# Kernel optimization log

Hardware: AMD Instinct MI355X
Metric: run time of the kernel (lower is better)

Reference implementation:

```python
import jax, jax.numpy as jnp
import numpy as np

NH = 8      # num_heads
KP = 3      # propagation_steps

def _ln(x, g, b, eps=1e-5):
    m = jnp.mean(x, -1, keepdims=True)
    v = jnp.mean(jnp.square(x - m), -1, keepdims=True)
    return (x - m) * jax.lax.rsqrt(v + eps) * g + b

def _mha(x, Wq, bq, Wk, bk, Wv, bv, Wo, bo):
    B, L, H = x.shape
    dh = H // NH
    q = (x @ Wq + bq).reshape(B, L, NH, dh)
    k = (x @ Wk + bk).reshape(B, L, NH, dh)
    v = (x @ Wv + bv).reshape(B, L, NH, dh)
    s = jnp.einsum('blhd,bmhd->bhlm', q, k) / jnp.sqrt(jnp.asarray(dh, x.dtype))
    p = jax.nn.softmax(s, axis=-1)
    o = jnp.einsum('bhlm,bmhd->blhd', p, v).reshape(B, L, H)
    return o @ Wo + bo

def setup_inputs():
    B, S, N, H = 2, 12, 800, 64
    keys = jax.random.split(jax.random.key(0), 64)
    it = iter(range(64))
    def nk():
        return keys[next(it)]
    def w(shape):
        return jax.random.normal(nk(), shape, jnp.float32) * 0.02
    p = {}
    p['x'] = jax.random.normal(nk(), (B, S, N, H), jnp.float32)
    # uniform weights scaled by 1/N (~row-normalized dense adjacency)
    p['adj'] = jax.random.uniform(nk(), (B, N, N), jnp.float32) / N
    p['W_gp'] = w((H, H)); p['b_gp'] = jnp.zeros((H,), jnp.float32)
    for sfx in ('s', 't'):
        for nm in ('Wq', 'Wk', 'Wv', 'Wo'):
            p[nm + '_' + sfx] = w((H, H))
        for nm in ('bq', 'bk', 'bv', 'bo'):
            p[nm + '_' + sfx] = jnp.zeros((H,), jnp.float32)
        p['g_' + sfx] = jnp.ones((H,), jnp.float32)
        p['be_' + sfx] = jnp.zeros((H,), jnp.float32)
    p['W1'] = w((H, 4 * H)); p['b1'] = jnp.zeros((4 * H,), jnp.float32)
    p['W2'] = w((4 * H, H)); p['b2'] = jnp.zeros((H,), jnp.float32)
    p['g1'] = jnp.ones((H,), jnp.float32); p['be1'] = jnp.zeros((H,), jnp.float32)
    p['g2'] = jnp.ones((H,), jnp.float32); p['be2'] = jnp.zeros((H,), jnp.float32)
    return p

def reference(x, adj, W_gp, b_gp,
              Wq_s, Wk_s, Wv_s, Wo_s, bq_s, bk_s, bv_s, bo_s, g_s, be_s,
              Wq_t, Wk_t, Wv_t, Wo_t, bq_t, bk_t, bv_t, bo_t, g_t, be_t,
              W1, b1, W2, b2, g1, be1, g2, be2):
    B, S, N, H = x.shape
    residual = x
    # accident-aware scaling (hidden_dim >= 6 path)
    acc = x[..., -2] * jnp.exp(-x[..., -1] / 60.0)
    xs = x * (1.0 + 0.3 * acc[..., None])
    # graph propagation: linear then K steps of relu(A @ h), vectorized over time
    h = xs @ W_gp + b_gp
    for _ in range(KP):
        h = jax.nn.relu(jnp.einsum('bnm,bsmh->bsnh', adj, h))
    prop = h + residual
    # spatial attention over nodes within each timestep
    xsa = prop.reshape(B * S, N, H)
    a = _mha(xsa, Wq_s, bq_s, Wk_s, bk_s, Wv_s, bv_s, Wo_s, bo_s)
    a = _ln(a + xsa, g_s, be_s).reshape(B, S, N, H)
    # temporal attention over timesteps per node
    xta = a.transpose(0, 2, 1, 3).reshape(B * N, S, H)
    t = _mha(xta, Wq_t, bq_t, Wk_t, bk_t, Wv_t, bv_t, Wo_t, bo_t)
    t = _ln(t + xta, g_t, be_t).reshape(B, N, S, H).transpose(0, 2, 1, 3)
    attn_out = t
    # pre-norm FFN with residual, post-norm output
    f = _ln(attn_out, g1, be1)
    f = jax.nn.relu(f @ W1 + b1) @ W2 + b2
    f = f + attn_out
    return _ln(f, g2, be2)
```

## Files before the change

kernel.cpp:

```cpp
#include <hip/hip_runtime.h>
#include <hip/hip_bf16.h>

#define NB 2
#define NS 12
#define NN 800
#define HEADS 8
#define DH 8
#define NBS (NB*NS)
#define NR (NB*NS*NN)

typedef __attribute__((ext_vector_type(4))) float f32x4;
typedef __attribute__((ext_vector_type(4))) short s16x4;
typedef __attribute__((ext_vector_type(8))) short s16x8;

static __device__ __forceinline__ unsigned short f2bf(float f) {
  union { float f; unsigned u; } v; v.f = f;
  unsigned r = (v.u + 0x7FFFu + ((v.u >> 16) & 1u)) >> 16;
  return (unsigned short)r;
}
static __device__ __forceinline__ float bf2f(unsigned short u) {
  union { unsigned u; float f; } v;
  v.u = ((unsigned)u) << 16;
  return v.f;
}
static __device__ __forceinline__ float fexp2(float x) {
  return __builtin_amdgcn_exp2f(x);
}
static __device__ __forceinline__ unsigned cvtpk_bf16(float a, float b) {
  unsigned r;
  asm("v_cvt_pk_bf16_f32 %0, %1, %2" : "=v"(r) : "v"(a), "v"(b));
  return r;
}

#define SC_LOG2 (0.35355339059327373f * 1.44269504088896f)

__global__ __launch_bounds__(256) void k_wconv(
    const float* __restrict__ w0, const float* __restrict__ w1,
    const float* __restrict__ w2, const float* __restrict__ w3,
    const float* __restrict__ w4, const float* __restrict__ w5,
    const float* __restrict__ w6, const float* __restrict__ w7,
    const float* __restrict__ w8, const float* __restrict__ W1,
    const float* __restrict__ W2, unsigned short* __restrict__ WB,
    unsigned short* __restrict__ W1B, unsigned short* __restrict__ W2B) {
  int i = blockIdx.x * 256 + threadIdx.x;
  if (i < 36864) {
    const float* ws[9] = {w0, w1, w2, w3, w4, w5, w6, w7, w8};
    WB[i] = f2bf(ws[i >> 12][i & 4095]);
  } else if (i < 53248) {
    W1B[i - 36864] = f2bf(W1[i - 36864]);
  } else if (i < 69632) {
    W2B[i - 53248] = f2bf(W2[i - 53248]);
  }
}

__global__ __launch_bounds__(256) void k_lin64T(
    const float* __restrict__ x, const unsigned short* __restrict__ Wb,
    const float* __restrict__ bias, unsigned short* __restrict__ HP) {
  __shared__ unsigned short As[32][36];
  __shared__ unsigned short Bs[64][36];
  const int tid = threadIdx.x;
  const int r0 = blockIdx.x * 32;
  const int w = tid >> 6, l = tid & 63;
  const int rb = (w & 1) * 16, cb = (w >> 1) * 32;
  f32x4 acc0 = {0.f, 0.f, 0.f, 0.f}, acc1 = {0.f, 0.f, 0.f, 0.f};
  const int ar = tid >> 3, ak = (tid & 7) * 4;
  const int bc = tid & 63, bm0 = (tid >> 6) * 4;
  const int k4 = (l >> 4) * 4;
  const int arow = rb + (l & 15);
  const int bcol0 = cb + (l & 15);
  const float* xrow = x + (size_t)(r0 + ar) * 64;
  float sf = 1.0f + 0.3f * xrow[62] * __expf(-xrow[63] * (1.0f / 60.0f));
  for (int k0 = 0; k0 < 64; k0 += 32) {
    __syncthreads();
    float4 xv = *(const float4*)(xrow + k0 + ak);
    ushort4 xb;
    xb.x = f2bf(xv.x * sf); xb.y = f2bf(xv.y * sf);
    xb.z = f2bf(xv.z * sf); xb.w = f2bf(xv.w * sf);
    *(ushort4*)&As[ar][ak] = xb;
#pragma unroll
    for (int j = 0; j < 4; ++j) {
      int mp = bm0 + j;
      unsigned lo = Wb[(size_t)(k0 + 2 * mp) * 64 + bc];
      unsigned hi = Wb[(size_t)(k0 + 2 * mp + 1) * 64 + bc];
      *(unsigned*)&Bs[bc][2 * mp] = lo | (hi << 16);
    }
    __syncthreads();
    s16x4 alo = *(const s16x4*)&As[arow][k4];
    s16x4 ahi = *(const s16x4*)&As[arow][k4 + 16];
    s16x8 a = {alo.x, alo.y, alo.z, alo.w, ahi.x, ahi.y, ahi.z, ahi.w};
    s16x4 b0l = *(const s16x4*)&Bs[bcol0][k4];
    s16x4 b0h = *(const s16x4*)&Bs[bcol0][k4 + 16];
    s16x8 bf0 = {b0l.x, b0l.y, b0l.z, b0l.w, b0h.x, b0h.y, b0h.z, b0h.w};
    s16x4 b1l = *(const s16x4*)&Bs[bcol0 + 16][k4];
    s16x4 b1h = *(const s16x4*)&Bs[bcol0 + 16][k4 + 16];
    s16x8 bf1 = {b1l.x, b1l.y, b1l.z, b1l.w, b1h.x, b1h.y, b1h.z, b1h.w};
    acc0 = __builtin_amdgcn_mfma_f32_16x16x32_bf16(a, bf0, acc0, 0, 0, 0);
    acc1 = __builtin_amdgcn_mfma_f32_16x16x32_bf16(a, bf1, acc1, 0, 0, 0);
  }
  const int c0 = cb + (l & 15);
  float b0 = bias[c0], b1 = bias[c0 + 16];
#pragma unroll
  for (int r = 0; r < 4; ++r) {
    int row = r0 + rb + (l >> 4) * 4 + r;
    int bs = row / NN, m = row % NN;
    HP[((size_t)bs * 64 + c0) * NN + m] = f2bf(acc0[r] + b0);
    HP[((size_t)bs * 64 + c0 + 16) * NN + m] = f2bf(acc1[r] + b1);
  }
}

template <bool LAST>
__global__ __launch_bounds__(256) void k_prop_mfma(
    const float* __restrict__ adj,
    const unsigned short* __restrict__ HPin,
    const float* __restrict__ x,
    unsigned short* __restrict__ HPout,
    float* __restrict__ pout,
    unsigned short* __restrict__ pbout) {
  __shared__ unsigned short As[32][36];
  __shared__ unsigned short Bs[64][40];
  const int tid = threadIdx.x;
  const int bid = blockIdx.x;
  const int bs = bid / 25, mt = bid % 25;
  const int b = bs / NS;
  const int n0 = mt * 32;
  const float* abase = adj + (size_t)b * NN * NN + (size_t)n0 * NN;
  const unsigned short* hbase = HPin + (size_t)bs * 64 * NN;
  const int w = tid >> 6, l = tid & 63;
  const int rb = (w & 1) * 16;
  const int cb = (w >> 1) * 32;
  f32x4 acc0 = {0.f, 0.f, 0.f, 0.f}, acc1 = {0.f, 0.f, 0.f, 0.f};
  const int ar = tid >> 3, ak = (tid & 7) * 4;
  const int bc = tid & 63, bq = tid >> 6;
  const int k4 = (l >> 4) * 4;
  const int arow = rb + (l & 15);
  const int bcol0 = cb + (l & 15);
  float4 av = *(const float4*)(abase + (size_t)ar * NN + ak);
  s16x8 bv = *(const s16x8*)(hbase + (size_t)bc * NN + bq * 8);
  for (int m0 = 0; m0 < NN; m0 += 32) {
    __syncthreads();
    {
      ushort4 ab;
      ab.x = f2bf(av.x); ab.y = f2bf(av.y);
      ab.z = f2bf(av.z); ab.w = f2bf(av.w);
      *(ushort4*)&As[ar][ak] = ab;
      *(s16x8*)&Bs[bc][bq * 8] = bv;
    }
    __syncthreads();
    if (m0 + 32 < NN) {
      av = *(const float4*)(abase + (size_t)ar * NN + m0 + 32 + ak);
      bv = *(const s16x8*)(hbase + (size_t)bc * NN + m0 + 32 + bq * 8);
    }
    s16x4 alo = *(const s16x4*)&As[arow][k4];
    s16x4 ahi = *(const s16x4*)&As[arow][k4 + 16];
    s16x8 a = {alo.x, alo.y, alo.z, alo.w, ahi.x, ahi.y, ahi.z, ahi.w};
    s16x4 b0l = *(const s16x4*)&Bs[bcol0][k4];
    s16x4 b0h = *(const s16x4*)&Bs[bcol0][k4 + 16];
    s16x8 bf0 = {b0l.x, b0l.y, b0l.z, b0l.w, b0h.x, b0h.y, b0h.z, b0h.w};
    s16x4 b1l = *(const s16x4*)&Bs[bcol0 + 16][k4];
    s16x4 b1h = *(const s16x4*)&Bs[bcol0 + 16][k4 + 16];
    s16x8 bf1 = {b1l.x, b1l.y, b1l.z, b1l.w, b1h.x, b1h.y, b1h.z, b1h.w};
    acc0 = __builtin_amdgcn_mfma_f32_16x16x32_bf16(a, bf0, acc0, 0, 0, 0);
    acc1 = __builtin_amdgcn_mfma_f32_16x16x32_bf16(a, bf1, acc1, 0, 0, 0);
  }
  const int c0 = cb + (l & 15);
  if (LAST) {
#pragma unroll
    for (int r = 0; r < 4; ++r) {
      int n = n0 + rb + (l >> 4) * 4 + r;
      float v0 = fmaxf(acc0[r], 0.f);
      float v1 = fmaxf(acc1[r], 0.f);
      size_t i0 = ((size_t)bs * NN + n) * 64 + c0;
      size_t i1 = i0 + 16;
      float p0 = v0 + x[i0], p1 = v1 + x[i1];
      pout[i0] = p0;
      pout[i1] = p1;
      pbout[i0] = f2bf(p0);
      pbout[i1] = f2bf(p1);
    }
  } else {
    int nb = n0 + rb + (l >> 4) * 4;
    s16x4 o0, o1;
#pragma unroll
    for (int r = 0; r < 4; ++r) {
      o0[r] = (short)f2bf(fmaxf(acc0[r], 0.f));
      o1[r] = (short)f2bf(fmaxf(acc1[r], 0.f));
    }
    *(s16x4*)&HPout[((size_t)bs * 64 + c0) * NN + nb] = o0;
    *(s16x4*)&HPout[((size_t)bs * 64 + c0 + 16) * NN + nb] = o1;
  }
}

__global__ __launch_bounds__(256) void k_qkv_mfma(
    const unsigned short* __restrict__ Xb,
    const unsigned short* __restrict__ Wq,
    const unsigned short* __restrict__ Wk,
    const unsigned short* __restrict__ Wv,
    const float* __restrict__ bq, const float* __restrict__ bk,
    const float* __restrict__ bv, float qscale,
    unsigned short* __restrict__ Qo, unsigned short* __restrict__ Ko,
    unsigned short* __restrict__ Vo) {
  __shared__ unsigned short As[32][36];
  __shared__ unsigned short Bs[3][64][36];
  const int tid = threadIdx.x;
  const int r0 = blockIdx.x * 32;
  const int w = tid >> 6, l = tid & 63;
  const int rb = (w & 1) * 16;
  const int cb = (w >> 1) * 32;
  f32x4 acc[3][2];
#pragma unroll
  for (int i = 0; i < 3; ++i)
#pragma unroll
    for (int j = 0; j < 2; ++j) acc[i][j] = (f32x4){0.f, 0.f, 0.f, 0.f};
  const unsigned short* Wm[3] = {Wq, Wk, Wv};
  const int ar = tid >> 3, ak = (tid & 7) * 4;
  const int bc = tid & 63, bm0 = (tid >> 6) * 4;
  const int k4 = (l >> 4) * 4;
  const int arow = rb + (l & 15);
  const int bcol0 = cb + (l & 15);
  for (int k0 = 0; k0 < 64; k0 += 32) {
    __syncthreads();
    *(s16x4*)&As[ar][ak] =
        *(const s16x4*)(Xb + (size_t)(r0 + ar) * 64 + k0 + ak);
#pragma unroll
    for (int wm = 0; wm < 3; ++wm) {
#pragma unroll
      for (int j = 0; j < 4; ++j) {
        int mp = bm0 + j;
        unsigned lo = Wm[wm][(size_t)(k0 + 2 * mp) * 64 + bc];
        unsigned hi = Wm[wm][(size_t)(k0 + 2 * mp + 1) * 64 + bc];
        *(unsigned*)&Bs[wm][bc][2 * mp] = lo | (hi << 16);
      }
    }
    __syncthreads();
    s16x4 alo = *(const s16x4*)&As[arow][k4];
    s16x4 ahi = *(const s16x4*)&As[arow][k4 + 16];
    s16x8 a = {alo.x, alo.y, alo.z, alo.w, ahi.x, ahi.y, ahi.z, ahi.w};
#pragma unroll
    for (int wm = 0; wm < 3; ++wm) {
      s16x4 b0l = *(const s16x4*)&Bs[wm][bcol0][k4];
      s16x4 b0h = *(const s16x4*)&Bs[wm][bcol0][k4 + 16];
      s16x8 bf0 = {b0l.x, b0l.y, b0l.z, b0l.w, b0h.x, b0h.y, b0h.z, b0h.w};
      s16x4 b1l = *(const s16x4*)&Bs[wm][bcol0 + 16][k4];
      s16x4 b1h = *(const s16x4*)&Bs[wm][bcol0 + 16][k4 + 16];
      s16x8 bf1 = {b1l.x, b1l.y, b1l.z, b1l.w, b1h.x, b1h.y, b1h.z, b1h.w};
      acc[wm][0] = __builtin_amdgcn_mfma_f32_16x16x32_bf16(a, bf0, acc[wm][0], 0, 0, 0);
      acc[wm][1] = __builtin_amdgcn_mfma_f32_16x16x32_bf16(a, bf1, acc[wm][1], 0, 0, 0);
    }
  }
  const float* bm[3] = {bq, bk, bv};
  unsigned short* Om[3] = {Qo, Ko, Vo};
  const int c0 = cb + (l & 15);
#pragma unroll
  for (int wm = 0; wm < 3; ++wm) {
    float b0 = bm[wm][c0], b1 = bm[wm][c0 + 16];
    float sc = (wm == 0) ? qscale : 1.0f;
#pragma unroll
    for (int r = 0; r < 4; ++r) {
      int row = r0 + rb + (l >> 4) * 4 + r;
      Om[wm][(size_t)row * 64 + c0] = f2bf((acc[wm][0][r] + b0) * sc);
      Om[wm][(size_t)row * 64 + c0 + 16] = f2bf((acc[wm][1][r] + b1) * sc);
    }
  }
}

__global__ __launch_bounds__(256) void k_sattn5(
    const unsigned short* __restrict__ Qb,
    const unsigned short* __restrict__ Kb,
    const unsigned short* __restrict__ Vb,
    unsigned short* __restrict__ OB) {
  __shared__ unsigned short Ks[800][8];
  __shared__ unsigned short Vt[25 * 256 + 256];
  const int bs = blockIdx.x, h = blockIdx.y;
  const int tid = threadIdx.x;
  const size_t base = (size_t)bs * NN * 64 + h * DH;
  for (int r = tid; r < NN; r += 256)
    *(s16x8*)&Ks[r][0] = *(const s16x8*)(Kb + base + (size_t)r * 64);
  if (tid < 200) {
    int t = tid >> 3, c = tid & 7;
    int r = t * 32 + c * 4;
    s16x8 v0 = *(const s16x8*)(Vb + base + (size_t)r * 64);
    s16x8 v1 = *(const s16x8*)(Vb + base + (size_t)(r + 1) * 64);
    s16x8 v2 = *(const s16x8*)(Vb + base + (size_t)(r + 2) * 64);
    s16x8 v3 = *(const s16x8*)(Vb + base + (size_t)(r + 3) * 64);
#pragma unroll
    for (int d = 0; d < 8; ++d) {
      unsigned lo = (unsigned short)v0[d] | ((unsigned)(unsigned short)v1[d] << 16);
      unsigned hi = (unsigned short)v2[d] | ((unsigned)(unsigned short)v3[d] << 16);
      unsigned* dst = (unsigned*)&Vt[t * 256 + d * 32 + ((c ^ d) & 7) * 4];
      dst[0] = lo;
      dst[1] = hi;
    }
  }
  __syncthreads();
  const int w = tid >> 6, l = tid & 63;
  const int q0 = blockIdx.z * 128 + w * 32;
  if (q0 >= NN) return;
  const int r15 = l & 15, g = l >> 4;
  const int dd = r15;
  const int off1 = dd * 32 + ((g ^ dd) & 7) * 4;
  const int off2 = dd * 32 + (((4 + g) ^ dd) & 7) * 4;
  s16x4 qvA = *(const s16x4*)(Qb + base + (size_t)(q0 + r15) * 64 + (g & 1) * 4);
  s16x4 qvB = *(const s16x4*)(Qb + base + (size_t)(q0 + 16 + r15) * 64 + (g & 1) * 4);
  s16x8 qfA = {0, 0, 0, 0, 0, 0, 0, 0};
  s16x8 qfB = {0, 0, 0, 0, 0, 0, 0, 0};
  if (g < 2) {
    qfA[0] = qvA.x; qfA[1] = qvA.y; qfA[2] = qvA.z; qfA[3] = qvA.w;
    qfB[0] = qvB.x; qfB[1] = qvB.y; qfB[2] = qvB.z; qfB[3] = qvB.w;
  }
  const short one_bf = (short)0x3F80;
  f32x4 accA = {0.f, 0.f, 0.f, 0.f}, accB = {0.f, 0.f, 0.f, 0.f};
  const f32x4 zero4 = {0.f, 0.f, 0.f, 0.f};
#pragma unroll 5
  for (int t = 0; t < 25; ++t) {
    s16x4 ka = *(const s16x4*)&Ks[t * 32 + r15][(g & 1) * 4];
    s16x4 kb = *(const s16x4*)&Ks[t * 32 + 16 + r15][(g & 1) * 4];
    s16x8 kfa = {0, 0, 0, 0, 0, 0, 0, 0};
    s16x8 kfb = {0, 0, 0, 0, 0, 0, 0, 0};
    if (g < 2) {
      kfa[0] = ka.x; kfa[1] = ka.y; kfa[2] = ka.z; kfa[3] = ka.w;
      kfb[0] = kb.x; kfb[1] = kb.y; kfb[2] = kb.z; kfb[3] = kb.w;
    }
    s16x4 va = *(const s16x4*)&Vt[t * 256 + off1];
    s16x4 vb = *(const s16x4*)&Vt[t * 256 + off2];
    s16x8 vf;
    if (dd < 8) {
      vf = (s16x8){va.x, va.y, va.z, va.w, vb.x, vb.y, vb.z, vb.w};
    } else if (dd == 8) {
      vf = (s16x8){one_bf, one_bf, one_bf, one_bf, one_bf, one_bf, one_bf, one_bf};
    } else {
      vf = (s16x8){0, 0, 0, 0, 0, 0, 0, 0};
    }
    f32x4 sA1 = __builtin_amdgcn_mfma_f32_16x16x32_bf16(kfa, qfA, zero4, 0, 0, 0);
    f32x4 sA2 = __builtin_amdgcn_mfma_f32_16x16x32_bf16(kfb, qfA, zero4, 0, 0, 0);
    f32x4 sB1 = __builtin_amdgcn_mfma_f32_16x16x32_bf16(kfa, qfB, zero4, 0, 0, 0);
    f32x4 sB2 = __builtin_amdgcn_mfma_f32_16x16x32_bf16(kfb, qfB, zero4, 0, 0, 0);
    float pA[8], pB[8];
#pragma unroll
    for (int r = 0; r < 4; ++r) {
      pA[r] = fexp2(sA1[r]);
      pA[4 + r] = fexp2(sA2[r]);
      pB[r] = fexp2(sB1[r]);
      pB[4 + r] = fexp2(sB2[r]);
    }
    union { unsigned u[4]; s16x8 v; } puA, puB;
    puA.u[0] = cvtpk_bf16(pA[0], pA[1]);
    puA.u[1] = cvtpk_bf16(pA[2], pA[3]);
    puA.u[2] = cvtpk_bf16(pA[4], pA[5]);
    puA.u[3] = cvtpk_bf16(pA[6], pA[7]);
    puB.u[0] = cvtpk_bf16(pB[0], pB[1]);
    puB.u[1] = cvtpk_bf16(pB[2], pB[3]);
    puB.u[2] = cvtpk_bf16(pB[4], pB[5]);
    puB.u[3] = cvtpk_bf16(pB[6], pB[7]);
    accA = __builtin_amdgcn_mfma_f32_16x16x32_bf16(vf, puA.v, accA, 0, 0, 0);
    accB = __builtin_amdgcn_mfma_f32_16x16x32_bf16(vf, puB.v, accB, 0, 0, 0);
  }
  float lsA = __shfl(accA[0], 32 + r15, 64);
  float lsB = __shfl(accB[0], 32 + r15, 64);
  float invA = 1.f / lsA;
  float invB = 1.f / lsB;
  if (g < 2) {
#pragma unroll
    for (int r = 0; r < 4; ++r) {
      int d = g * 4 + r;
      OB[base + (size_t)(q0 + r15) * 64 + d] = f2bf(accA[r] * invA);
      OB[base + (size_t)(q0 + 16 + r15) * 64 + d] = f2bf(accB[r] * invB);
    }
  }
}

template <bool LN2>
__global__ __launch_bounds__(256) void k_projln_mfma(
    const unsigned short* __restrict__ Xb,
    const unsigned short* __restrict__ Wb,
    const float* __restrict__ bias, const float* __restrict__ res,
    const float* __restrict__ g, const float* __restrict__ be,
    const float* __restrict__ g2, const float* __restrict__ be2,
    float* __restrict__ out, unsigned short* __restrict__ bfout) {
  __shared__ unsigned short As[32][36];
  __shared__ unsigned short Bs[64][36];
  __shared__ float CT[32][68];
  const int tid = threadIdx.x;
  const int r0 = blockIdx.x * 32;
  const int w = tid >> 6, l = tid & 63;
  const int rb = (w & 1) * 16, cb = (w >> 1) * 32;
  f32x4 acc0 = {0.f, 0.f, 0.f, 0.f}, acc1 = {0.f, 0.f, 0.f, 0.f};
  const int ar = tid >> 3, ak = (tid & 7) * 4;
  const int bc = tid & 63, bm0 = (tid >> 6) * 4;
  const int k4 = (l >> 4) * 4;
  const int arow = rb + (l & 15);
  const int bcol0 = cb + (l & 15);
  for (int k0 = 0; k0 < 64; k0 += 32) {
    __syncthreads();
    *(s16x4*)&As[ar][ak] = *(const s16x4*)(Xb + (size_t)(r0 + ar) * 64 + k0 + ak);
#pragma unroll
    for (int j = 0; j < 4; ++j) {
      int mp = bm0 + j;
      unsigned lo = Wb[(size_t)(k0 + 2 * mp) * 64 + bc];
      unsigned hi = Wb[(size_t)(k0 + 2 * mp + 1) * 64 + bc];
      *(unsigned*)&Bs[bc][2 * mp] = lo | (hi << 16);
    }
    __syncthreads();
    s16x4 alo = *(const s16x4*)&As[arow][k4];
    s16x4 ahi = *(const s16x4*)&As[arow][k4 + 16];
    s16x8 a = {alo.x, alo.y, alo.z, alo.w, ahi.x, ahi.y, ahi.z, ahi.w};
    s16x4 b0l = *(const s16x4*)&Bs[bcol0][k4];
    s16x4 b0h = *(const s16x4*)&Bs[bcol0][k4 + 16];
    s16x8 bf0 = {b0l.x, b0l.y, b0l.z, b0l.w, b0h.x, b0h.y, b0h.z, b0h.w};
    s16x4 b1l = *(const s16x4*)&Bs[bcol0 + 16][k4];
    s16x4 b1h = *(const s16x4*)&Bs[bcol0 + 16][k4 + 16];
    s16x8 bf1 = {b1l.x, b1l.y, b1l.z, b1l.w, b1h.x, b1h.y, b1h.z, b1h.w};
    acc0 = __builtin_amdgcn_mfma_f32_16x16x32_bf16(a, bf0, acc0, 0, 0, 0);
    acc1 = __builtin_amdgcn_mfma_f32_16x16x32_bf16(a, bf1, acc1, 0, 0, 0);
  }
  const int c0 = cb + (l & 15);
#pragma unroll
  for (int r = 0; r < 4; ++r) {
    int row = rb + (l >> 4) * 4 + r;
    size_t gi = (size_t)(r0 + row) * 64;
    CT[row][c0] = acc0[r] + bias[c0] + res[gi + c0];
    CT[row][c0 + 16] = acc1[r] + bias[c0 + 16] + res[gi + c0 + 16];
  }
  __syncthreads();
  const int row = tid >> 3, sub = tid & 7;
  float v[8];
#pragma unroll
  for (int i = 0; i < 8; ++i) v[i] = CT[row][sub * 8 + i];
  float s = 0.f;
#pragma unroll
  for (int i = 0; i < 8; ++i) s += v[i];
#pragma unroll
  for (int off = 1; off < 8; off <<= 1) s += __shfl_xor(s, off, 64);
  float mean = s * (1.f / 64.f);
  float q = 0.f;
#pragma unroll
  for (int i = 0; i < 8; ++i) {
    float ddd = v[i] - mean;
    q += ddd * ddd;
  }
#pragma unroll
  for (int off = 1; off < 8; off <<= 1) q += __shfl_xor(q, off, 64);
  float rstd = rsqrtf(q * (1.f / 64.f) + 1e-5f);
  float r4[8];
#pragma unroll
  for (int i = 0; i < 8; ++i)
    r4[i] = (v[i] - mean) * rstd * g[sub * 8 + i] + be[sub * 8 + i];
  float* op = out + (size_t)(r0 + row) * 64 + sub * 8;
  *(float4*)op = (float4){r4[0], r4[1], r4[2], r4[3]};
  *(float4*)(op + 4) = (float4){r4[4], r4[5], r4[6], r4[7]};
  unsigned short* bp = bfout + (size_t)(r0 + row) * 64 + sub * 8;
  if (!LN2) {
#pragma unroll
    for (int i = 0; i < 8; ++i) bp[i] = f2bf(r4[i]);
  } else {
    float s2 = 0.f;
#pragma unroll
    for (int i = 0; i < 8; ++i) s2 += r4[i];
#pragma unroll
    for (int off = 1; off < 8; off <<= 1) s2 += __shfl_xor(s2, off, 64);
    float mean2 = s2 * (1.f / 64.f);
    float q2 = 0.f;
#pragma unroll
    for (int i = 0; i < 8; ++i) {
      float d2 = r4[i] - mean2;
      q2 += d2 * d2;
    }
#pragma unroll
    for (int off = 1; off < 8; off <<= 1) q2 += __shfl_xor(q2, off, 64);
    float rstd2 = rsqrtf(q2 * (1.f / 64.f) + 1e-5f);
#pragma unroll
    for (int i = 0; i < 8; ++i)
      bp[i] = f2bf((r4[i] - mean2) * rstd2 * g2[sub * 8 + i] + be2[sub * 8 + i]);
  }
}

__global__ __launch_bounds__(256) void k_tattn(
    const unsigned short* __restrict__ Q, const unsigned short* __restrict__ K,
    const unsigned short* __restrict__ V, unsigned short* __restrict__ O) {
  int b = blockIdx.x / NN, n = blockIdx.x % NN;
  __shared__ float Qs[12][64], Ks[12][64], Vs[12][64];
  int tid = threadIdx.x;
  for (int i = tid; i < 12 * 64; i += 256) {
    int s = i >> 6, c = i & 63;
    size_t idx = (((size_t)b * NS + s) * NN + n) * 64 + c;
    Qs[s][c] = bf2f(Q[idx]);
    Ks[s][c] = bf2f(K[idx]);
    Vs[s][c] = bf2f(V[idx]);
  }
  __syncthreads();
  for (int wi = tid; wi < 12 * 64; wi += 256) {
    int l = wi >> 6, c = wi & 63;
    int h8 = c & 56;
    float sc[12];
    float mx = -1e30f;
#pragma unroll
    for (int m = 0; m < 12; ++m) {
      float s = 0.f;
#pragma unroll
      for (int d = 0; d < 8; ++d) s += Qs[l][h8 + d] * Ks[m][h8 + d];
      s *= 0.35355339059327373f;
      sc[m] = s;
      mx = fmaxf(mx, s);
    }
    float sum = 0.f;
#pragma unroll
    for (int m = 0; m < 12; ++m) {
      sc[m] = __expf(sc[m] - mx);
      sum += sc[m];
    }
    float inv = 1.f / sum;
    float o = 0.f;
#pragma unroll
    for (int m = 0; m < 12; ++m) o += sc[m] * Vs[m][c];
    size_t idx = (((size_t)b * NS + l) * NN + n) * 64 + c;
    O[idx] = f2bf(o * inv);
  }
}

__global__ __launch_bounds__(256) void k_ffn_fused(
    const unsigned short* __restrict__ Xb,
    const unsigned short* __restrict__ W1b,
    const float* __restrict__ b1,
    const unsigned short* __restrict__ W2b,
    const float* __restrict__ b2,
    const float* __restrict__ res,
    const float* __restrict__ g, const float* __restrict__ be,
    float* __restrict__ out) {
  __shared__ unsigned short As[32][68];
  __shared__ unsigned short Bs[64][66];
  __shared__ unsigned short Hs[32][264];
  __shared__ float CT[32][68];
  const int tid = threadIdx.x;
  const int r0 = blockIdx.x * 32;
  const int w = tid >> 6, l = tid & 63;
  const int rb = (w & 1) * 16, cb = (w >> 1) * 32;
  const int r15 = l & 15;
  const int k4 = (l >> 4) * 4;
  const int arow = rb + r15;
  const int bcol0 = cb + r15;
  {
    int ar = tid >> 3, ak8 = (tid & 7) * 8;
    *(s16x8*)&As[ar][ak8] = *(const s16x8*)(Xb + (size_t)(r0 + ar) * 64 + ak8);
  }
  const int sbc = tid & 63;
  for (int c = 0; c < 4; ++c) {
    __syncthreads();
    {
      const int smp0 = (tid >> 6) * 8;
      int gcol = c * 64 + sbc;
#pragma unroll
      for (int j = 0; j < 8; ++j) {
        int mp = smp0 + j;
        unsigned lo = W1b[(size_t)(2 * mp) * 256 + gcol];
        unsigned hi = W1b[(size_t)(2 * mp + 1) * 256 + gcol];
        *(unsigned*)&Bs[sbc][2 * mp] = lo | (hi << 16);
      }
    }
    __syncthreads();
    f32x4 acc0 = {0.f, 0.f, 0.f, 0.f}, acc1 = {0.f, 0.f, 0.f, 0.f};
#pragma unroll
    for (int k0 = 0; k0 < 64; k0 += 32) {
      s16x4 alo = *(const s16x4*)&As[arow][k0 + k4];
      s16x4 ahi = *(const s16x4*)&As[arow][k0 + k4 + 16];
      s16x8 a = {alo.x, alo.y, alo.z, alo.w, ahi.x, ahi.y, ahi.z, ahi.w};
      s16x4 b0l = *(const s16x4*)&Bs[bcol0][k0 + k4];
      s16x4 b0h = *(const s16x4*)&Bs[bcol0][k0 + k4 + 16];
      s16x8 bf0 = {b0l.x, b0l.y, b0l.z, b0l.w, b0h.x, b0h.y, b0h.z, b0h.w};
      s16x4 b1l = *(const s16x4*)&Bs[bcol0 + 16][k0 + k4];
      s16x4 b1h = *(const s16x4*)&Bs[bcol0 + 16][k0 + k4 + 16];
      s16x8 bf1 = {b1l.x, b1l.y, b1l.z, b1l.w, b1h.x, b1h.y, b1h.z, b1h.w};
      acc0 = __builtin_amdgcn_mfma_f32_16x16x32_bf16(a, bf0, acc0, 0, 0, 0);
      acc1 = __builtin_amdgcn_mfma_f32_16x16x32_bf16(a, bf1, acc1, 0, 0, 0);
    }
    int c0 = cb + r15;
    float bb0 = b1[c * 64 + c0], bb1v = b1[c * 64 + c0 + 16];
#pragma unroll
    for (int r = 0; r < 4; ++r) {
      int row = rb + (l >> 4) * 4 + r;
      Hs[row][c * 64 + c0] = f2bf(fmaxf(acc0[r] + bb0, 0.f));
      Hs[row][c * 64 + c0 + 16] = f2bf(fmaxf(acc1[r] + bb1v, 0.f));
    }
  }
  f32x4 acc0 = {0.f, 0.f, 0.f, 0.f}, acc1 = {0.f, 0.f, 0.f, 0.f};
  const int smp4 = (tid >> 6) * 4;
  for (int k0 = 0; k0 < 256; k0 += 32) {
    __syncthreads();
#pragma unroll
    for (int j = 0; j < 4; ++j) {
      int mp = smp4 + j;
      unsigned lo = W2b[(size_t)(k0 + 2 * mp) * 64 + sbc];
      unsigned hi = W2b[(size_t)(k0 + 2 * mp + 1) * 64 + sbc];
      *(unsigned*)&Bs[sbc][2 * mp] = lo | (hi << 16);
    }
    __syncthreads();
    s16x4 alo = *(const s16x4*)&Hs[arow][k0 + k4];
    s16x4 ahi = *(const s16x4*)&Hs[arow][k0 + k4 + 16];
    s16x8 a = {alo.x, alo.y, alo.z, alo.w, ahi.x, ahi.y, ahi.z, ahi.w};
    s16x4 b0l = *(const s16x4*)&Bs[bcol0][k4];
    s16x4 b0h = *(const s16x4*)&Bs[bcol0][k4 + 16];
    s16x8 bf0 = {b0l.x, b0l.y, b0l.z, b0l.w, b0h.x, b0h.y, b0h.z, b0h.w};
    s16x4 b1l = *(const s16x4*)&Bs[bcol0 + 16][k4];
    s16x4 b1h = *(const s16x4*)&Bs[bcol0 + 16][k4 + 16];
    s16x8 bf1 = {b1l.x, b1l.y, b1l.z, b1l.w, b1h.x, b1h.y, b1h.z, b1h.w};
    acc0 = __builtin_amdgcn_mfma_f32_16x16x32_bf16(a, bf0, acc0, 0, 0, 0);
    acc1 = __builtin_amdgcn_mfma_f32_16x16x32_bf16(a, bf1, acc1, 0, 0, 0);
  }
  const int c0 = cb + r15;
#pragma unroll
  for (int r = 0; r < 4; ++r) {
    int row = rb + (l >> 4) * 4 + r;
    size_t gi = (size_t)(r0 + row) * 64;
    CT[row][c0] = acc0[r] + b2[c0] + res[gi + c0];
    CT[row][c0 + 16] = acc1[r] + b2[c0 + 16] + res[gi + c0 + 16];
  }
  __syncthreads();
  const int row = tid >> 3, sub = tid & 7;
  float v[8];
#pragma unroll
  for (int i = 0; i < 8; ++i) v[i] = CT[row][sub * 8 + i];
  float s = 0.f;
#pragma unroll
  for (int i = 0; i < 8; ++i) s += v[i];
#pragma unroll
  for (int off = 1; off < 8; off <<= 1) s += __shfl_xor(s, off, 64);
  float mean = s * (1.f / 64.f);
  float q = 0.f;
#pragma unroll
  for (int i = 0; i < 8; ++i) {
    float d = v[i] - mean;
    q += d * d;
  }
#pragma unroll
  for (int off = 1; off < 8; off <<= 1) q += __shfl_xor(q, off, 64);
  float rstd = rsqrtf(q * (1.f / 64.f) + 1e-5f);
  float r4[8];
#pragma unroll
  for (int i = 0; i < 8; ++i)
    r4[i] = (v[i] - mean) * rstd * g[sub * 8 + i] + be[sub * 8 + i];
  float* op = out + (size_t)(r0 + row) * 64 + sub * 8;
  *(float4*)op = (float4){r4[0], r4[1], r4[2], r4[3]};
  *(float4*)(op + 4) = (float4){r4[4], r4[5], r4[6], r4[7]};
}

extern "C" void kernel_launch(void* const* d_in, const int* in_sizes, int n_in,
                              void* d_out, int out_size, void* d_ws,
                              size_t ws_size, hipStream_t stream) {
  const float* x = (const float*)d_in[0];
  const float* adj = (const float*)d_in[1];
  const float* W_gp = (const float*)d_in[2];
  const float* b_gp = (const float*)d_in[3];
  const float* Wq_s = (const float*)d_in[4];
  const float* Wk_s = (const float*)d_in[5];
  const float* Wv_s = (const float*)d_in[6];
  const float* Wo_s = (const float*)d_in[7];
  const float* bq_s = (const float*)d_in[8];
  const float* bk_s = (const float*)d_in[9];
  const float* bv_s = (const float*)d_in[10];
  const float* bo_s = (const float*)d_in[11];
  const float* g_s = (const float*)d_in[12];
  const float* be_s = (const float*)d_in[13];
  const float* Wq_t = (const float*)d_in[14];
  const float* Wk_t = (const float*)d_in[15];
  const float* Wv_t = (const float*)d_in[16];
  const float* Wo_t = (const float*)d_in[17];
  const float* bq_t = (const float*)d_in[18];
  const float* bk_t = (const float*)d_in[19];
  const float* bv_t = (const float*)d_in[20];
  const float* bo_t = (const float*)d_in[21];
  const float* g_t = (const float*)d_in[22];
  const float* be_t = (const float*)d_in[23];
  const float* W1 = (const float*)d_in[24];
  const float* b1 = (const float*)d_in[25];
  const float* W2 = (const float*)d_in[26];
  const float* b2 = (const float*)d_in[27];
  const float* g1 = (const float*)d_in[28];
  const float* be1 = (const float*)d_in[29];
  const float* g2 = (const float*)d_in[30];
  const float* be2 = (const float*)d_in[31];
  float* out = (float*)d_out;

  float* ws = (float*)d_ws;
  const size_t U = (size_t)NR * 64;
  float* A = ws + 0 * U;
  float* Bb = ws + 1 * U;
  float* C = ws + 2 * U;
  float* D = ws + 3 * U;
  float* P = ws + 4 * U;
  unsigned short* QB = (unsigned short*)A;
  unsigned short* KB = (unsigned short*)Bb;
  unsigned short* VB = (unsigned short*)C;
  unsigned short* OBuf = (unsigned short*)D;
  unsigned short* Q2 = (unsigned short*)C;
  unsigned short* K2 = (unsigned short*)D;
  unsigned short* V2 = (unsigned short*)(ws + 5 * U + U);
  unsigned short* PB = (unsigned short*)(ws + 5 * U);
  unsigned short* LNB = (unsigned short*)(ws + 7 * U);
  unsigned short* TB = LNB;
  unsigned short* W1B = (unsigned short*)(ws + 7 * U + U / 2);
  unsigned short* W2B = W1B + 16384;
  unsigned short* HP0 = (unsigned short*)(ws + 9 * U);
  unsigned short* HP1 = (unsigned short*)(ws + 9 * U + U / 2);
  unsigned short* WB = (unsigned short*)(ws + 10 * U + 650240);

  dim3 blk(256);
  k_wconv<<<272, blk, 0, stream>>>(Wq_s, Wk_s, Wv_s, Wq_t, Wk_t, Wv_t, W_gp,
                                   Wo_s, Wo_t, W1, W2, WB, W1B, W2B);
  k_lin64T<<<NR / 32, blk, 0, stream>>>(x, WB + 6 * 4096, b_gp, HP0);
  k_prop_mfma<false><<<NBS * 25, blk, 0, stream>>>(adj, HP0, x, HP1, P, PB);
  k_prop_mfma<false><<<NBS * 25, blk, 0, stream>>>(adj, HP1, x, HP0, P, PB);
  k_prop_mfma<true><<<NBS * 25, blk, 0, stream>>>(adj, HP0, x, HP1, P, PB);
  k_qkv_mfma<<<NR / 32, blk, 0, stream>>>(PB, WB, WB + 4096, WB + 8192, bq_s,
                                          bk_s, bv_s, SC_LOG2, QB, KB, VB);
  k_sattn5<<<dim3(NBS, HEADS, 7), blk, 0, stream>>>(QB, KB, VB, OBuf);
  k_projln_mfma<false><<<NR / 32, blk, 0, stream>>>(
      OBuf, WB + 7 * 4096, bo_s, P, g_s, be_s, nullptr, nullptr, A, PB);
  k_qkv_mfma<<<NR / 32, blk, 0, stream>>>(PB, WB + 12288, WB + 16384,
                                          WB + 20480, bq_t, bk_t, bv_t, 1.0f,
                                          Q2, K2, V2);
  k_tattn<<<NB * NN, blk, 0, stream>>>(Q2, K2, V2, TB);
  k_projln_mfma<true><<<NR / 32, blk, 0, stream>>>(
      TB, WB + 8 * 4096, bo_t, A, g_t, be_t, g1, be1, Bb, LNB);
  k_ffn_fused<<<NR / 32, blk, 0, stream>>>(LNB, W1B, b1, W2B, b2, Bb, g2, be2,
                                           out);
}
```

Baseline: 150.7 us.

## Fuse spatial out-proj+LN with temporal QKV, and temporal out-proj+LN with FFN

```diff
diff --git a/kernel.cpp b/kernel.cpp
--- a/kernel.cpp
+++ b/kernel.cpp
@@ -368,108 +368,135 @@
   }
 }
 
-template <bool LN2>
-__global__ __launch_bounds__(256) void k_projln_mfma(
-    const unsigned short* __restrict__ Xb,
-    const unsigned short* __restrict__ Wb,
-    const float* __restrict__ bias, const float* __restrict__ res,
-    const float* __restrict__ g, const float* __restrict__ be,
-    const float* __restrict__ g2, const float* __restrict__ be2,
-    float* __restrict__ out, unsigned short* __restrict__ bfout) {
-  __shared__ unsigned short As[32][36];
-  __shared__ unsigned short Bs[64][36];
+__global__ __launch_bounds__(256) void k_sproj_tqkv(
+    const unsigned short* __restrict__ OBuf,
+    const unsigned short* __restrict__ WoS, const float* __restrict__ boS,
+    const float* __restrict__ res, const float* __restrict__ gS,
+    const float* __restrict__ beS,
+    const unsigned short* __restrict__ Wq,
+    const unsigned short* __restrict__ Wk,
+    const unsigned short* __restrict__ Wv,
+    const float* __restrict__ bq, const float* __restrict__ bk,
+    const float* __restrict__ bv,
+    float* __restrict__ Aout, unsigned short* __restrict__ Qo,
+    unsigned short* __restrict__ Ko, unsigned short* __restrict__ Vo) {
+  __shared__ unsigned short Xs[32][68];
+  __shared__ unsigned short Bs[64][68];
   __shared__ float CT[32][68];
   const int tid = threadIdx.x;
   const int r0 = blockIdx.x * 32;
   const int w = tid >> 6, l = tid & 63;
   const int rb = (w & 1) * 16, cb = (w >> 1) * 32;
+  const int r15 = l & 15;
+  const int k4 = (l >> 4) * 4;
+  const int arow = rb + r15;
+  const int bcol0 = cb + r15;
+  const int c0 = cb + r15;
+  {
+    int ar = tid >> 3, ak8 = (tid & 7) * 8;
+    *(s16x8*)&Xs[ar][ak8] = *(const s16x8*)(OBuf + (size_t)(r0 + ar) * 64 + ak8);
+    int bc = tid & 63, bm0 = (tid >> 6) * 8;
+#pragma unroll
+    for (int j = 0; j < 8; ++j) {
+      int mp = bm0 + j;
+      unsigned lo = WoS[(size_t)(2 * mp) * 64 + bc];
+      unsigned hi = WoS[(size_t)(2 * mp + 1) * 64 + bc];
+      *(unsigned*)&Bs[bc][2 * mp] = lo | (hi << 16);
+    }
+  }
+  __syncthreads();
   f32x4 acc0 = {0.f, 0.f, 0.f, 0.f}, acc1 = {0.f, 0.f, 0.f, 0.f};
-  const int ar = tid >> 3, ak = (tid & 7) * 4;
-  const int bc = tid & 63, bm0 = (tid >> 6) * 4;
-  const int k4 = (l >> 4) * 4;
-  const int arow = rb + (l & 15);
-  const int bcol0 = cb + (l & 15);
+#pragma unroll
   for (int k0 = 0; k0 < 64; k0 += 32) {
-    __syncthreads();
-    *(s16x4*)&As[ar][ak] = *(const s16x4*)(Xb + (size_t)(r0 + ar) * 64 + k0 + ak);
-#pragma unroll
-    for (int j = 0; j < 4; ++j) {
-      int mp = bm0 + j;
-      unsigned lo = Wb[(size_t)(k0 + 2 * mp) * 64 + bc];
-      unsigned hi = Wb[(size_t)(k0 + 2 * mp + 1) * 64 + bc];
-      *(unsigned*)&Bs[bc][2 * mp] = lo | (hi << 16);
-    }
-    __syncthreads();
-    s16x4 alo = *(const s16x4*)&As[arow][k4];
-    s16x4 ahi = *(const s16x4*)&As[arow][k4 + 16];
+    s16x4 alo = *(const s16x4*)&Xs[arow][k0 + k4];
+    s16x4 ahi = *(const s16x4*)&Xs[arow][k0 + k4 + 16];
     s16x8 a = {alo.x, alo.y, alo.z, alo.w, ahi.x, ahi.y, ahi.z, ahi.w};
-    s16x4 b0l = *(const s16x4*)&Bs[bcol0][k4];
-    s16x4 b0h = *(const s16x4*)&Bs[bcol0][k4 + 16];
+    s16x4 b0l = *(const s16x4*)&Bs[bcol0][k0 + k4];
+    s16x4 b0h = *(const s16x4*)&Bs[bcol0][k0 + k4 + 16];
     s16x8 bf0 = {b0l.x, b0l.y, b0l.z, b0l.w, b0h.x, b0h.y, b0h.z, b0h.w};
-    s16x4 b1l = *(const s16x4*)&Bs[bcol0 + 16][k4];
-    s16x4 b1h = *(const s16x4*)&Bs[bcol0 + 16][k4 + 16];
+    s16x4 b1l = *(const s16x4*)&Bs[bcol0 + 16][k0 + k4];
+    s16x4 b1h = *(const s16x4*)&Bs[bcol0 + 16][k0 + k4 + 16];
     s16x8 bf1 = {b1l.x, b1l.y, b1l.z, b1l.w, b1h.x, b1h.y, b1h.z, b1h.w};
     acc0 = __builtin_amdgcn_mfma_f32_16x16x32_bf16(a, bf0, acc0, 0, 0, 0);
     acc1 = __builtin_amdgcn_mfma_f32_16x16x32_bf16(a, bf1, acc1, 0, 0, 0);
   }
-  const int c0 = cb + (l & 15);
 #pragma unroll
   for (int r = 0; r < 4; ++r) {
     int row = rb + (l >> 4) * 4 + r;
     size_t gi = (size_t)(r0 + row) * 64;
-    CT[row][c0] = acc0[r] + bias[c0] + res[gi + c0];
-    CT[row][c0 + 16] = acc1[r] + bias[c0 + 16] + res[gi + c0 + 16];
+    CT[row][c0] = acc0[r] + boS[c0] + res[gi + c0];
+    CT[row][c0 + 16] = acc1[r] + boS[c0 + 16] + res[gi + c0 + 16];
   }
   __syncthreads();
-  const int row = tid >> 3, sub = tid & 7;
-  float v[8];
-#pragma unroll
-  for (int i = 0; i < 8; ++i) v[i] = CT[row][sub * 8 + i];
-  float s = 0.f;
-#pragma unroll
-  for (int i = 0; i < 8; ++i) s += v[i];
-#pragma unroll
-  for (int off = 1; off < 8; off <<= 1) s += __shfl_xor(s, off, 64);
-  float mean = s * (1.f / 64.f);
-  float q = 0.f;
-#pragma unroll
-  for (int i = 0; i < 8; ++i) {
-    float ddd = v[i] - mean;
-    q += ddd * ddd;
-  }
-#pragma unroll
-  for (int off = 1; off < 8; off <<= 1) q += __shfl_xor(q, off, 64);
-  float rstd = rsqrtf(q * (1.f / 64.f) + 1e-5f);
-  float r4[8];
-#pragma unroll
-  for (int i = 0; i < 8; ++i)
-    r4[i] = (v[i] - mean) * rstd * g[sub * 8 + i] + be[sub * 8 + i];
-  float* op = out + (size_t)(r0 + row) * 64 + sub * 8;
-  *(float4*)op = (float4){r4[0], r4[1], r4[2], r4[3]};
-  *(float4*)(op + 4) = (float4){r4[4], r4[5], r4[6], r4[7]};
-  unsigned short* bp = bfout + (size_t)(r0 + row) * 64 + sub * 8;
-  if (!LN2) {
-#pragma unroll
-    for (int i = 0; i < 8; ++i) bp[i] = f2bf(r4[i]);
-  } else {
-    float s2 = 0.f;
-#pragma unroll
-    for (int i = 0; i < 8; ++i) s2 += r4[i];
-#pragma unroll
-    for (int off = 1; off < 8; off <<= 1) s2 += __shfl_xor(s2, off, 64);
-    float mean2 = s2 * (1.f / 64.f);
-    float q2 = 0.f;
+  {
+    const int row = tid >> 3, sub = tid & 7;
+    float v[8];
+#pragma unroll
+    for (int i = 0; i < 8; ++i) v[i] = CT[row][sub * 8 + i];
+    float s = 0.f;
+#pragma unroll
+    for (int i = 0; i < 8; ++i) s += v[i];
+#pragma unroll
+    for (int off = 1; off < 8; off <<= 1) s += __shfl_xor(s, off, 64);
+    float mean = s * (1.f / 64.f);
+    float q = 0.f;
 #pragma unroll
     for (int i = 0; i < 8; ++i) {
-      float d2 = r4[i] - mean2;
-      q2 += d2 * d2;
-    }
-#pragma unroll
-    for (int off = 1; off < 8; off <<= 1) q2 += __shfl_xor(q2, off, 64);
-    float rstd2 = rsqrtf(q2 * (1.f / 64.f) + 1e-5f);
+      float d = v[i] - mean;
+      q += d * d;
+    }
+#pragma unroll
+    for (int off = 1; off < 8; off <<= 1) q += __shfl_xor(q, off, 64);
+    float rstd = rsqrtf(q * (1.f / 64.f) + 1e-5f);
+    float r4[8];
 #pragma unroll
     for (int i = 0; i < 8; ++i)
-      bp[i] = f2bf((r4[i] - mean2) * rstd2 * g2[sub * 8 + i] + be2[sub * 8 + i]);
+      r4[i] = (v[i] - mean) * rstd * gS[sub * 8 + i] + beS[sub * 8 + i];
+    float* op = Aout + (size_t)(r0 + row) * 64 + sub * 8;
+    *(float4*)op = (float4){r4[0], r4[1], r4[2], r4[3]};
+    *(float4*)(op + 4) = (float4){r4[4], r4[5], r4[6], r4[7]};
+#pragma unroll
+    for (int i = 0; i < 8; ++i) Xs[row][sub * 8 + i] = f2bf(r4[i]);
+  }
+  const unsigned short* Wm[3] = {Wq, Wk, Wv};
+  const float* bm[3] = {bq, bk, bv};
+  unsigned short* Om[3] = {Qo, Ko, Vo};
+#pragma unroll 1
+  for (int wm = 0; wm < 3; ++wm) {
+    __syncthreads();
+    {
+      int bc = tid & 63, bm0 = (tid >> 6) * 8;
+#pragma unroll
+      for (int j = 0; j < 8; ++j) {
+        int mp = bm0 + j;
+        unsigned lo = Wm[wm][(size_t)(2 * mp) * 64 + bc];
+        unsigned hi = Wm[wm][(size_t)(2 * mp + 1) * 64 + bc];
+        *(unsigned*)&Bs[bc][2 * mp] = lo | (hi << 16);
+      }
+    }
+    __syncthreads();
+    f32x4 q0a = {0.f, 0.f, 0.f, 0.f}, q1a = {0.f, 0.f, 0.f, 0.f};
+#pragma unroll
+    for (int k0 = 0; k0 < 64; k0 += 32) {
+      s16x4 alo = *(const s16x4*)&Xs[arow][k0 + k4];
+      s16x4 ahi = *(const s16x4*)&Xs[arow][k0 + k4 + 16];
+      s16x8 a = {alo.x, alo.y, alo.z, alo.w, ahi.x, ahi.y, ahi.z, ahi.w};
+      s16x4 b0l = *(const s16x4*)&Bs[bcol0][k0 + k4];
+      s16x4 b0h = *(const s16x4*)&Bs[bcol0][k0 + k4 + 16];
+      s16x8 bf0 = {b0l.x, b0l.y, b0l.z, b0l.w, b0h.x, b0h.y, b0h.z, b0h.w};
+      s16x4 b1l = *(const s16x4*)&Bs[bcol0 + 16][k0 + k4];
+      s16x4 b1h = *(const s16x4*)&Bs[bcol0 + 16][k0 + k4 + 16];
+      s16x8 bf1 = {b1l.x, b1l.y, b1l.z, b1l.w, b1h.x, b1h.y, b1h.z, b1h.w};
+      q0a = __builtin_amdgcn_mfma_f32_16x16x32_bf16(a, bf0, q0a, 0, 0, 0);
+      q1a = __builtin_amdgcn_mfma_f32_16x16x32_bf16(a, bf1, q1a, 0, 0, 0);
+    }
+    float b0 = bm[wm][c0], b1 = bm[wm][c0 + 16];
+#pragma unroll
+    for (int r = 0; r < 4; ++r) {
+      int row = r0 + rb + (l >> 4) * 4 + r;
+      Om[wm][(size_t)row * 64 + c0] = f2bf(q0a[r] + b0);
+      Om[wm][(size_t)row * 64 + c0 + 16] = f2bf(q1a[r] + b1);
+    }
   }
 }
 
@@ -516,19 +543,20 @@
   }
 }
 
-__global__ __launch_bounds__(256) void k_ffn_fused(
-    const unsigned short* __restrict__ Xb,
-    const unsigned short* __restrict__ W1b,
-    const float* __restrict__ b1,
-    const unsigned short* __restrict__ W2b,
-    const float* __restrict__ b2,
-    const float* __restrict__ res,
-    const float* __restrict__ g, const float* __restrict__ be,
+__global__ __launch_bounds__(256) void k_tproj_ffn(
+    const unsigned short* __restrict__ TBin,
+    const unsigned short* __restrict__ WoT, const float* __restrict__ boT,
+    const float* __restrict__ resA, const float* __restrict__ gT,
+    const float* __restrict__ beT, const float* __restrict__ g1,
+    const float* __restrict__ be1,
+    const unsigned short* __restrict__ W1b, const float* __restrict__ b1,
+    const unsigned short* __restrict__ W2b, const float* __restrict__ b2,
+    const float* __restrict__ g2, const float* __restrict__ be2,
     float* __restrict__ out) {
-  __shared__ unsigned short As[32][68];
-  __shared__ unsigned short Bs[64][66];
+  __shared__ unsigned short Xs[32][68];
+  __shared__ unsigned short Bs[64][68];
+  __shared__ float CT[32][68];
   __shared__ unsigned short Hs[32][264];
-  __shared__ float CT[32][68];
   const int tid = threadIdx.x;
   const int r0 = blockIdx.x * 32;
   const int w = tid >> 6, l = tid & 63;
@@ -537,30 +565,27 @@
   const int k4 = (l >> 4) * 4;
   const int arow = rb + r15;
   const int bcol0 = cb + r15;
+  const int c0 = cb + r15;
+  const int sbc = tid & 63;
   {
     int ar = tid >> 3, ak8 = (tid & 7) * 8;
-    *(s16x8*)&As[ar][ak8] = *(const s16x8*)(Xb + (size_t)(r0 + ar) * 64 + ak8);
-  }
-  const int sbc = tid & 63;
-  for (int c = 0; c < 4; ++c) {
-    __syncthreads();
-    {
-      const int smp0 = (tid >> 6) * 8;
-      int gcol = c * 64 + sbc;
-#pragma unroll
-      for (int j = 0; j < 8; ++j) {
-        int mp = smp0 + j;
-        unsigned lo = W1b[(size_t)(2 * mp) * 256 + gcol];
-        unsigned hi = W1b[(size_t)(2 * mp + 1) * 256 + gcol];
-        *(unsigned*)&Bs[sbc][2 * mp] = lo | (hi << 16);
-      }
-    }
-    __syncthreads();
+    *(s16x8*)&Xs[ar][ak8] = *(const s16x8*)(TBin + (size_t)(r0 + ar) * 64 + ak8);
+    int bm0 = (tid >> 6) * 8;
+#pragma unroll
+    for (int j = 0; j < 8; ++j) {
+      int mp = bm0 + j;
+      unsigned lo = WoT[(size_t)(2 * mp) * 64 + sbc];
+      unsigned hi = WoT[(size_t)(2 * mp + 1) * 64 + sbc];
+      *(unsigned*)&Bs[sbc][2 * mp] = lo | (hi << 16);
+    }
+  }
+  __syncthreads();
+  {
     f32x4 acc0 = {0.f, 0.f, 0.f, 0.f}, acc1 = {0.f, 0.f, 0.f, 0.f};
 #pragma unroll
     for (int k0 = 0; k0 < 64; k0 += 32) {
-      s16x4 alo = *(const s16x4*)&As[arow][k0 + k4];
-      s16x4 ahi = *(const s16x4*)&As[arow][k0 + k4 + 16];
+      s16x4 alo = *(const s16x4*)&Xs[arow][k0 + k4];
+      s16x4 ahi = *(const s16x4*)&Xs[arow][k0 + k4 + 16];
       s16x8 a = {alo.x, alo.y, alo.z, alo.w, ahi.x, ahi.y, ahi.z, ahi.w};
       s16x4 b0l = *(const s16x4*)&Bs[bcol0][k0 + k4];
       s16x4 b0h = *(const s16x4*)&Bs[bcol0][k0 + k4 + 16];
@@ -571,7 +596,90 @@
       acc0 = __builtin_amdgcn_mfma_f32_16x16x32_bf16(a, bf0, acc0, 0, 0, 0);
       acc1 = __builtin_amdgcn_mfma_f32_16x16x32_bf16(a, bf1, acc1, 0, 0, 0);
     }
-    int c0 = cb + r15;
+#pragma unroll
+    for (int r = 0; r < 4; ++r) {
+      int row = rb + (l >> 4) * 4 + r;
+      size_t gi = (size_t)(r0 + row) * 64;
+      CT[row][c0] = acc0[r] + boT[c0] + resA[gi + c0];
+      CT[row][c0 + 16] = acc1[r] + boT[c0 + 16] + resA[gi + c0 + 16];
+    }
+  }
+  __syncthreads();
+  {
+    const int row = tid >> 3, sub = tid & 7;
+    float v[8];
+#pragma unroll
+    for (int i = 0; i < 8; ++i) v[i] = CT[row][sub * 8 + i];
+    float s = 0.f;
+#pragma unroll
+    for (int i = 0; i < 8; ++i) s += v[i];
+#pragma unroll
+    for (int off = 1; off < 8; off <<= 1) s += __shfl_xor(s, off, 64);
+    float mean = s * (1.f / 64.f);
+    float q = 0.f;
+#pragma unroll
+    for (int i = 0; i < 8; ++i) {
+      float d = v[i] - mean;
+      q += d * d;
+    }
+#pragma unroll
+    for (int off = 1; off < 8; off <<= 1) q += __shfl_xor(q, off, 64);
+    float rstd = rsqrtf(q * (1.f / 64.f) + 1e-5f);
+    float r4[8];
+#pragma unroll
+    for (int i = 0; i < 8; ++i)
+      r4[i] = (v[i] - mean) * rstd * gT[sub * 8 + i] + beT[sub * 8 + i];
+#pragma unroll
+    for (int i = 0; i < 8; ++i) CT[row][sub * 8 + i] = r4[i];
+    float s2 = 0.f;
+#pragma unroll
+    for (int i = 0; i < 8; ++i) s2 += r4[i];
+#pragma unroll
+    for (int off = 1; off < 8; off <<= 1) s2 += __shfl_xor(s2, off, 64);
+    float mean2 = s2 * (1.f / 64.f);
+    float q2 = 0.f;
+#pragma unroll
+    for (int i = 0; i < 8; ++i) {
+      float d2 = r4[i] - mean2;
+      q2 += d2 * d2;
+    }
+#pragma unroll
+    for (int off = 1; off < 8; off <<= 1) q2 += __shfl_xor(q2, off, 64);
+    float rstd2 = rsqrtf(q2 * (1.f / 64.f) + 1e-5f);
+#pragma unroll
+    for (int i = 0; i < 8; ++i)
+      Xs[row][sub * 8 + i] =
+          f2bf((r4[i] - mean2) * rstd2 * g1[sub * 8 + i] + be1[sub * 8 + i]);
+  }
+  __syncthreads();
+  for (int c = 0; c < 4; ++c) {
+    {
+      const int bm0 = (tid >> 6) * 8;
+      int gcol = c * 64 + sbc;
+#pragma unroll
+      for (int j = 0; j < 8; ++j) {
+        int mp = bm0 + j;
+        unsigned lo = W1b[(size_t)(2 * mp) * 256 + gcol];
+        unsigned hi = W1b[(size_t)(2 * mp + 1) * 256 + gcol];
+        *(unsigned*)&Bs[sbc][2 * mp] = lo | (hi << 16);
+      }
+    }
+    __syncthreads();
+    f32x4 acc0 = {0.f, 0.f, 0.f, 0.f}, acc1 = {0.f, 0.f, 0.f, 0.f};
+#pragma unroll
+    for (int k0 = 0; k0 < 64; k0 += 32) {
+      s16x4 alo = *(const s16x4*)&Xs[arow][k0 + k4];
+      s16x4 ahi = *(const s16x4*)&Xs[arow][k0 + k4 + 16];
+      s16x8 a = {alo.x, alo.y, alo.z, alo.w, ahi.x, ahi.y, ahi.z, ahi.w};
+      s16x4 b0l = *(const s16x4*)&Bs[bcol0][k0 + k4];
+      s16x4 b0h = *(const s16x4*)&Bs[bcol0][k0 + k4 + 16];
+      s16x8 bf0 = {b0l.x, b0l.y, b0l.z, b0l.w, b0h.x, b0h.y, b0h.z, b0h.w};
+      s16x4 b1l = *(const s16x4*)&Bs[bcol0 + 16][k0 + k4];
+      s16x4 b1h = *(const s16x4*)&Bs[bcol0 + 16][k0 + k4 + 16];
+      s16x8 bf1 = {b1l.x, b1l.y, b1l.z, b1l.w, b1h.x, b1h.y, b1h.z, b1h.w};
+      acc0 = __builtin_amdgcn_mfma_f32_16x16x32_bf16(a, bf0, acc0, 0, 0, 0);
+      acc1 = __builtin_amdgcn_mfma_f32_16x16x32_bf16(a, bf1, acc1, 0, 0, 0);
+    }
     float bb0 = b1[c * 64 + c0], bb1v = b1[c * 64 + c0 + 16];
 #pragma unroll
     for (int r = 0; r < 4; ++r) {
@@ -579,11 +687,11 @@
       Hs[row][c * 64 + c0] = f2bf(fmaxf(acc0[r] + bb0, 0.f));
       Hs[row][c * 64 + c0 + 16] = f2bf(fmaxf(acc1[r] + bb1v, 0.f));
     }
+    __syncthreads();
   }
   f32x4 acc0 = {0.f, 0.f, 0.f, 0.f}, acc1 = {0.f, 0.f, 0.f, 0.f};
   const int smp4 = (tid >> 6) * 4;
   for (int k0 = 0; k0 < 256; k0 += 32) {
-    __syncthreads();
 #pragma unroll
     for (int j = 0; j < 4; ++j) {
       int mp = smp4 + j;
@@ -603,42 +711,43 @@
     s16x8 bf1 = {b1l.x, b1l.y, b1l.z, b1l.w, b1h.x, b1h.y, b1h.z, b1h.w};
     acc0 = __builtin_amdgcn_mfma_f32_16x16x32_bf16(a, bf0, acc0, 0, 0, 0);
     acc1 = __builtin_amdgcn_mfma_f32_16x16x32_bf16(a, bf1, acc1, 0, 0, 0);
-  }
-  const int c0 = cb + r15;
+    __syncthreads();
+  }
 #pragma unroll
   for (int r = 0; r < 4; ++r) {
     int row = rb + (l >> 4) * 4 + r;
-    size_t gi = (size_t)(r0 + row) * 64;
-    CT[row][c0] = acc0[r] + b2[c0] + res[gi + c0];
-    CT[row][c0 + 16] = acc1[r] + b2[c0 + 16] + res[gi + c0 + 16];
+    CT[row][c0] = acc0[r] + b2[c0] + CT[row][c0];
+    CT[row][c0 + 16] = acc1[r] + b2[c0 + 16] + CT[row][c0 + 16];
   }
   __syncthreads();
-  const int row = tid >> 3, sub = tid & 7;
-  float v[8];
-#pragma unroll
-  for (int i = 0; i < 8; ++i) v[i] = CT[row][sub * 8 + i];
-  float s = 0.f;
-#pragma unroll
-  for (int i = 0; i < 8; ++i) s += v[i];
-#pragma unroll
-  for (int off = 1; off < 8; off <<= 1) s += __shfl_xor(s, off, 64);
-  float mean = s * (1.f / 64.f);
-  float q = 0.f;
-#pragma unroll
-  for (int i = 0; i < 8; ++i) {
-    float d = v[i] - mean;
-    q += d * d;
-  }
-#pragma unroll
-  for (int off = 1; off < 8; off <<= 1) q += __shfl_xor(q, off, 64);
-  float rstd = rsqrtf(q * (1.f / 64.f) + 1e-5f);
-  float r4[8];
-#pragma unroll
-  for (int i = 0; i < 8; ++i)
-    r4[i] = (v[i] - mean) * rstd * g[sub * 8 + i] + be[sub * 8 + i];
-  float* op = out + (size_t)(r0 + row) * 64 + sub * 8;
-  *(float4*)op = (float4){r4[0], r4[1], r4[2], r4[3]};
-  *(float4*)(op + 4) = (float4){r4[4], r4[5], r4[6], r4[7]};
+  {
+    const int row = tid >> 3, sub = tid & 7;
+    float v[8];
+#pragma unroll
+    for (int i = 0; i < 8; ++i) v[i] = CT[row][sub * 8 + i];
+    float s = 0.f;
+#pragma unroll
+    for (int i = 0; i < 8; ++i) s += v[i];
+#pragma unroll
+    for (int off = 1; off < 8; off <<= 1) s += __shfl_xor(s, off, 64);
+    float mean = s * (1.f / 64.f);
+    float q = 0.f;
+#pragma unroll
+    for (int i = 0; i < 8; ++i) {
+      float d = v[i] - mean;
+      q += d * d;
+    }
+#pragma unroll
+    for (int off = 1; off < 8; off <<= 1) q += __shfl_xor(q, off, 64);
+    float rstd = rsqrtf(q * (1.f / 64.f) + 1e-5f);
+    float r4[8];
+#pragma unroll
+    for (int i = 0; i < 8; ++i)
+      r4[i] = (v[i] - mean) * rstd * g2[sub * 8 + i] + be2[sub * 8 + i];
+    float* op = out + (size_t)(r0 + row) * 64 + sub * 8;
+    *(float4*)op = (float4){r4[0], r4[1], r4[2], r4[3]};
+    *(float4*)(op + 4) = (float4){r4[4], r4[5], r4[6], r4[7]};
+  }
 }
 
 extern "C" void kernel_launch(void* const* d_in, const int* in_sizes, int n_in,
@@ -681,20 +790,16 @@
   float* ws = (float*)d_ws;
   const size_t U = (size_t)NR * 64;
   float* A = ws + 0 * U;
-  float* Bb = ws + 1 * U;
-  float* C = ws + 2 * U;
-  float* D = ws + 3 * U;
   float* P = ws + 4 * U;
-  unsigned short* QB = (unsigned short*)A;
-  unsigned short* KB = (unsigned short*)Bb;
-  unsigned short* VB = (unsigned short*)C;
-  unsigned short* OBuf = (unsigned short*)D;
-  unsigned short* Q2 = (unsigned short*)C;
-  unsigned short* K2 = (unsigned short*)D;
-  unsigned short* V2 = (unsigned short*)(ws + 5 * U + U);
+  unsigned short* QB = (unsigned short*)(ws + 0 * U);
+  unsigned short* KB = (unsigned short*)(ws + 1 * U);
+  unsigned short* VB = (unsigned short*)(ws + 2 * U);
+  unsigned short* OBuf = (unsigned short*)(ws + 3 * U);
+  unsigned short* Q2 = (unsigned short*)(ws + 1 * U);
+  unsigned short* K2 = (unsigned short*)(ws + 6 * U);
+  unsigned short* V2 = K2 + (size_t)NR * 64;
   unsigned short* PB = (unsigned short*)(ws + 5 * U);
-  unsigned short* LNB = (unsigned short*)(ws + 7 * U);
-  unsigned short* TB = LNB;
+  unsigned short* TB = (unsigned short*)(ws + 7 * U);
   unsigned short* W1B = (unsigned short*)(ws + 7 * U + U / 2);
   unsigned short* W2B = W1B + 16384;
   unsigned short* HP0 = (unsigned short*)(ws + 9 * U);
@@ -711,14 +816,12 @@
   k_qkv_mfma<<<NR / 32, blk, 0, stream>>>(PB, WB, WB + 4096, WB + 8192, bq_s,
                                           bk_s, bv_s, SC_LOG2, QB, KB, VB);
   k_sattn5<<<dim3(NBS, HEADS, 7), blk, 0, stream>>>(QB, KB, VB, OBuf);
-  k_projln_mfma<false><<<NR / 32, blk, 0, stream>>>(
-      OBuf, WB + 7 * 4096, bo_s, P, g_s, be_s, nullptr, nullptr, A, PB);
-  k_qkv_mfma<<<NR / 32, blk, 0, stream>>>(PB, WB + 12288, WB + 16384,
-                                          WB + 20480, bq_t, bk_t, bv_t, 1.0f,
-                                          Q2, K2, V2);
+  k_sproj_tqkv<<<NR / 32, blk, 0, stream>>>(OBuf, WB + 7 * 4096, bo_s, P, g_s,
+                                            be_s, WB + 12288, WB + 16384,
+                                            WB + 20480, bq_t, bk_t, bv_t, A, Q2,
+                                            K2, V2);
   k_tattn<<<NB * NN, blk, 0, stream>>>(Q2, K2, V2, TB);
-  k_projln_mfma<true><<<NR / 32, blk, 0, stream>>>(
-      TB, WB + 8 * 4096, bo_t, A, g_t, be_t, g1, be1, Bb, LNB);
-  k_ffn_fused<<<NR / 32, blk, 0, stream>>>(LNB, W1B, b1, W2B, b2, Bb, g2, be2,
-                                           out);
-}
+  k_tproj_ffn<<<NR / 32, blk, 0, stream>>>(TB, WB + 8 * 4096, bo_t, A, g_t,
+                                           be_t, g1, be1, W1B, b1, W2B, b2, g2,
+                                           be2, out);
+}
```

Result: faster. 136.7 us (-9.3%).
